# Kernel optimization log

Measured on AMD Instinct MI355X. Metric: run time of the kernel, lower is better.

## Reference

```python
import jax, jax.numpy as jnp
import numpy as np

BN_EPS = 1e-3  # keras BatchNormalization default epsilon


def setup_inputs() -> dict:
    key = jax.random.key(0)
    ks = jax.random.split(key, 7)
    B, W, D, H, C = 2, 32, 32, 32, 256
    x = jax.random.normal(ks[0], (B, W, D, H, C), dtype=jnp.float32)
    # Stacked params for the 4 branches: [query, key, judge, value]
    conv_w = jax.random.normal(ks[1], (4, C, C), dtype=jnp.float32) / np.sqrt(C).astype(np.float32)
    conv_b = jax.random.normal(ks[2], (4, C), dtype=jnp.float32) * 0.01
    bn_scale = 1.0 + 0.1 * jax.random.normal(ks[3], (4, C), dtype=jnp.float32)
    bn_offset = 0.1 * jax.random.normal(ks[4], (4, C), dtype=jnp.float32)
    bn_mean = 0.1 * jax.random.normal(ks[5], (4, C), dtype=jnp.float32)
    bn_var = jax.random.uniform(ks[6], (4, C), dtype=jnp.float32, minval=0.5, maxval=1.5)
    gamma = jnp.asarray(1e-4, dtype=jnp.float32)  # scalar residual scale (init 0.0001 in source)
    return dict(x=x, conv_w=conv_w, conv_b=conv_b, bn_scale=bn_scale,
                bn_offset=bn_offset, bn_mean=bn_mean, bn_var=bn_var, gamma=gamma)


def _branch(x, w, b, s, o, m, v):
    # Conv3D 1x1x1 == per-voxel channel mixing, then inference-mode BN, then ReLU
    y = jnp.einsum('bwdhc,cf->bwdhf', x, w) + b
    y = s * (y - m) * jax.lax.rsqrt(v + BN_EPS) + o
    return jax.nn.relu(y)


def reference(x, conv_w, conv_b, bn_scale, bn_offset, bn_mean, bn_var, gamma):
    B, W, D, H, C = x.shape
    N = W * D * H
    # Raw reshape (B,W,D,H,C) -> (B,C,N), matching keras Reshape((C,-1)) on channels-last layout
    def br(i):
        return _branch(x, conv_w[i], conv_b[i], bn_scale[i], bn_offset[i],
                       bn_mean[i], bn_var[i]).reshape(B, C, N)
    Q, K, J, V = br(0), br(1), br(2), br(3)
    m1 = jnp.matmul(K, jnp.swapaxes(Q, 1, 2))   # (B, C, C)
    m2 = jnp.matmul(K, jnp.swapaxes(J, 1, 2))   # (B, C, C)
    affinity = jax.nn.sigmoid(jnp.matmul(m1, m2))  # (B, C, C), sigmoid not softmax
    weights = jnp.matmul(affinity, V)           # (B, C, N)
    weights = weights.reshape(B, W, D, H, C)    # raw reshape back, as in source
    return gamma * weights + x
```

## Files before the change

### kernel.cpp

```cpp
#include <hip/hip_runtime.h>
#include <math.h>

typedef __attribute__((ext_vector_type(4))) float  f32x4;
typedef __attribute__((ext_vector_type(8))) short  s16x8;
typedef __attribute__((ext_vector_type(4))) short  s16x4;

#define BN_EPS 1e-3f

static constexpr int    CC    = 256;
static constexpr int    NVOX  = 32768;
static constexpr int    BATCH = 2;
static constexpr int    MTOT  = BATCH * NVOX;
static constexpr size_t ELEM_BR = (size_t)MTOT * CC;
static constexpr size_t SZ_BR   = ELEM_BR * 2;
static constexpr size_t WS_Q   = 0;
static constexpr size_t WS_K   = WS_Q  + SZ_BR;
static constexpr size_t WS_J   = WS_K  + SZ_BR;
static constexpr size_t WS_V   = WS_J  + SZ_BR;
static constexpr size_t WS_M1  = WS_V  + SZ_BR;
static constexpr size_t WS_M2  = WS_M1 + (size_t)BATCH*CC*CC*4;
static constexpr size_t WS_AFF = WS_M2 + (size_t)BATCH*CC*CC*4;
static constexpr size_t WS_WT  = WS_AFF + (size_t)BATCH*CC*CC*2;
static constexpr size_t WS_AB  = WS_WT + (size_t)4*CC*CC*2;

__device__ __forceinline__ short f2bf(float f) {
  union { float f; unsigned u; } v; v.f = f;
  unsigned u = v.u + 0x7FFFu + ((v.u >> 16) & 1u);
  return (short)(u >> 16);
}

__global__ __launch_bounds__(256) void k0_prep(
    const float* __restrict__ conv_w, const float* __restrict__ conv_b,
    const float* __restrict__ bn_s, const float* __restrict__ bn_o,
    const float* __restrict__ bn_m, const float* __restrict__ bn_v,
    char* __restrict__ ws)
{
  int t = blockIdx.x * 256 + threadIdx.x;
  ((float*)(ws + WS_M1))[t] = 0.f;
  int f = t >> 16, rem = t & 65535;
  int cin = rem >> 8, cout = rem & 255;
  ((short*)(ws + WS_WT))[f*65536 + cout*256 + cin] = f2bf(conv_w[t]);
  if (t < 1024) {
    float alpha = bn_s[t] * rsqrtf(bn_v[t] + BN_EPS);
    float beta  = alpha * (conv_b[t] - bn_m[t]) + bn_o[t];
    float* ab = (float*)(ws + WS_AB);
    ab[t] = alpha; ab[1024 + t] = beta;
  }
}

__global__ __launch_bounds__(256, 2) void k1_branches(
    const float* __restrict__ x, char* __restrict__ ws)
{
  __shared__ short As[64 * 256];
  __shared__ short Bs[64 * 256];
  __shared__ short Rs[64][72];

  const int tid = threadIdx.x;
  const int m0  = blockIdx.x * 64;
  const int lane = tid & 63, wid = tid >> 6;
  const int wm = wid >> 1, wn = wid & 1;
  const int lr = lane & 15, lg = lane >> 4;

  const short* Wt = (const short*)(ws + WS_WT);
  const float* ab = (const float*)(ws + WS_AB);

  #pragma unroll
  for (int it = 0; it < 16; ++it) {
    int idx = tid + 256 * it;
    int r = idx >> 6, c4 = (idx & 63) << 2;
    const float4 v = *(const float4*)(x + (size_t)(m0 + r) * 256 + c4);
    s16x4 s; s[0]=f2bf(v.x); s[1]=f2bf(v.y); s[2]=f2bf(v.z); s[3]=f2bf(v.w);
    int u = c4 >> 3;
    int swz = ((u ^ ((r & 7) << 2)) << 3) | (c4 & 7);
    *(s16x4*)&As[r * 256 + swz] = s;
  }

  {
    const short* Wf = Wt;
    #pragma unroll
    for (int i = 0; i < 8; ++i) {
      int slot = i * 256 + tid;
      int cout = slot >> 5, u = slot & 31;
      int usrc = u ^ ((cout & 7) << 2);
      const short* src = Wf + cout * 256 + usrc * 8;
      short* dst = Bs + (size_t)(i * 256 + wid * 64) * 8;
      __builtin_amdgcn_global_load_lds(
          (const __attribute__((address_space(1))) void*)src,
          (__attribute__((address_space(3))) void*)dst, 16, 0, 0);
    }
  }

  __syncthreads();

  for (int nt = 0; nt < 16; ++nt) {
    const int f  = nt >> 2;
    const int c0 = (nt & 3) * 64;

    f32x4 acc[2][2];
    #pragma unroll
    for (int a = 0; a < 2; ++a)
      #pragma unroll
      for (int b = 0; b < 2; ++b) { f32x4 z = {0.f,0.f,0.f,0.f}; acc[a][b] = z; }

    #pragma unroll
    for (int k0 = 0; k0 < 8; ++k0) {
      const int ua = k0 * 4 + lg;
      s16x8 af[2], bf[2];
      #pragma unroll
      for (int mi = 0; mi < 2; ++mi) {
        int r = wm*32 + mi*16 + lr;
        int uu = ua ^ ((r & 7) << 2);
        af[mi] = *(const s16x8*)&As[r * 256 + uu * 8];
      }
      #pragma unroll
      for (int nj = 0; nj < 2; ++nj) {
        int c = wn*32 + nj*16 + lr;
        int uu = ua ^ ((c & 7) << 2);
        bf[nj] = *(const s16x8*)&Bs[c * 256 + uu * 8];
      }
      #pragma unroll
      for (int mi = 0; mi < 2; ++mi)
        #pragma unroll
        for (int nj = 0; nj < 2; ++nj)
          acc[mi][nj] = __builtin_amdgcn_mfma_f32_16x16x32_bf16(
              bf[nj], af[mi], acc[mi][nj], 0, 0, 0);
    }

    __syncthreads();

    if (nt < 15) {
      const int fn  = (nt + 1) >> 2;
      const int c0n = ((nt + 1) & 3) * 64;
      const short* Wf = Wt + fn * 65536 + c0n * 256;
      #pragma unroll
      for (int i = 0; i < 8; ++i) {
        int slot = i * 256 + tid;
        int cout = slot >> 5, u = slot & 31;
        int usrc = u ^ ((cout & 7) << 2);
        const short* src = Wf + cout * 256 + usrc * 8;
        short* dst = Bs + (size_t)(i * 256 + wid * 64) * 8;
        __builtin_amdgcn_global_load_lds(
            (const __attribute__((address_space(1))) void*)src,
            (__attribute__((address_space(3))) void*)dst, 16, 0, 0);
      }
    }

    #pragma unroll
    for (int nj = 0; nj < 2; ++nj) {
      int c4b = c0 + wn*32 + nj*16 + lg*4;
      const f32x4 al = *(const f32x4*)&ab[f*256 + c4b];
      const f32x4 be = *(const f32x4*)&ab[1024 + f*256 + c4b];
      #pragma unroll
      for (int mi = 0; mi < 2; ++mi) {
        s16x4 s;
        #pragma unroll
        for (int ii = 0; ii < 4; ++ii) {
          float yv = al[ii] * acc[mi][nj][ii] + be[ii];
          yv = yv > 0.f ? yv : 0.f;
          s[ii] = f2bf(yv);
        }
        *(s16x4*)&Rs[wm*32 + mi*16 + lr][wn*32 + nj*16 + lg*4] = s;
      }
    }

    __syncthreads();

    short* Yf = (short*)(ws + (size_t)f * SZ_BR);
    #pragma unroll
    for (int it = 0; it < 2; ++it) {
      int idx = tid + 256 * it;
      int r = idx >> 3, c8 = (idx & 7) << 3;
      *(s16x8*)&Yf[(size_t)(m0 + r) * 256 + c0 + c8] = *(const s16x8*)&Rs[r][c8];
    }
  }
}

__global__ __launch_bounds__(256, 2) void k2_m1m2(char* __restrict__ ws)
{
  __shared__ short Ks[128][88], Qs[128][88], Js[128][88];

  const int tid = threadIdx.x;
  const int chunk = blockIdx.x;
  const int ti = blockIdx.y >> 1, tj = blockIdx.y & 1;
  const int b  = blockIdx.z;
  const size_t boff = (size_t)b * NVOX * CC;
  const short* Qm = (const short*)(ws + WS_Q) + boff;
  const short* Km = (const short*)(ws + WS_K) + boff;
  const short* Jm = (const short*)(ws + WS_J) + boff;

  const int lane = tid & 63, wid = tid >> 6;
  const int wm = wid >> 1, wn = wid & 1;
  const int lr = lane & 15, lg = lane >> 4;

  f32x4 accq[4][4], accj[4][4];
  #pragma unroll
  for (int a = 0; a < 4; ++a)
    #pragma unroll
    for (int c = 0; c < 4; ++c) { f32x4 z = {0.f,0.f,0.f,0.f}; accq[a][c] = z; accj[a][c] = z; }

  const int nstart = chunk * 1024;
  for (int n0 = nstart; n0 < nstart + 1024; n0 += 64) {
    __syncthreads();
    #pragma unroll
    for (int it = 0; it < 4; ++it) {
      int idx = tid + 256 * it;
      int r = idx >> 3, n8 = (idx & 7) << 3;
      *(s16x8*)&Ks[r][n8] = *(const s16x8*)&Km[(size_t)(ti*128 + r)*NVOX + n0 + n8];
      *(s16x8*)&Qs[r][n8] = *(const s16x8*)&Qm[(size_t)(tj*128 + r)*NVOX + n0 + n8];
      *(s16x8*)&Js[r][n8] = *(const s16x8*)&Jm[(size_t)(tj*128 + r)*NVOX + n0 + n8];
    }
    __syncthreads();
    #pragma unroll
    for (int ks = 0; ks < 2; ++ks) {
      s16x8 a[4], bq[4], bj[4];
      #pragma unroll
      for (int mi = 0; mi < 4; ++mi)
        a[mi] = *(const s16x8*)&Ks[wm*64 + mi*16 + lr][ks*32 + lg*8];
      #pragma unroll
      for (int nj = 0; nj < 4; ++nj) {
        bq[nj] = *(const s16x8*)&Qs[wn*64 + nj*16 + lr][ks*32 + lg*8];
        bj[nj] = *(const s16x8*)&Js[wn*64 + nj*16 + lr][ks*32 + lg*8];
      }
      #pragma unroll
      for (int mi = 0; mi < 4; ++mi)
        #pragma unroll
        for (int nj = 0; nj < 4; ++nj) {
          accq[mi][nj] = __builtin_amdgcn_mfma_f32_16x16x32_bf16(a[mi], bq[nj], accq[mi][nj], 0,0,0);
          accj[mi][nj] = __builtin_amdgcn_mfma_f32_16x16x32_bf16(a[mi], bj[nj], accj[mi][nj], 0,0,0);
        }
    }
  }
  float* m1 = (float*)(ws + WS_M1) + (size_t)b * CC * CC;
  float* m2 = (float*)(ws + WS_M2) + (size_t)b * CC * CC;
  #pragma unroll
  for (int mi = 0; mi < 4; ++mi)
    #pragma unroll
    for (int nj = 0; nj < 4; ++nj)
      #pragma unroll
      for (int ii = 0; ii < 4; ++ii) {
        int i = ti*128 + wm*64 + mi*16 + lg*4 + ii;
        int j = tj*128 + wn*64 + nj*16 + lr;
        atomicAdd(&m1[i*256 + j], accq[mi][nj][ii]);
        atomicAdd(&m2[i*256 + j], accj[mi][nj][ii]);
      }
}

__global__ __launch_bounds__(256) void k3_aff(char* __restrict__ ws)
{
  const int j = threadIdx.x;
  const int i = blockIdx.x & 255;
  const int b = blockIdx.x >> 8;
  const float* m1 = (const float*)(ws + WS_M1) + (size_t)b * CC * CC;
  const float* m2 = (const float*)(ws + WS_M2) + (size_t)b * CC * CC;
  float z = 0.f;
  #pragma unroll 8
  for (int k = 0; k < 256; ++k)
    z = fmaf(m1[i*256 + k], m2[k*256 + j], z);
  float a = 1.f / (1.f + expf(-z));
  ((short*)(ws + WS_AFF))[(size_t)b*CC*CC + i*256 + j] = f2bf(a);
}

__global__ __launch_bounds__(512, 4) void k4_out(
    const float* __restrict__ x, const float* __restrict__ gamma_p,
    char* __restrict__ ws, float* __restrict__ out)
{
  __shared__ short affS[256][72];
  __shared__ short Vs[128][72];

  const int tid = threadIdx.x;
  const int n0 = blockIdx.x * 128;
  const int b  = blockIdx.y;
  const float gamma = gamma_p[0];
  const short* aff = (const short*)(ws + WS_AFF) + (size_t)b * CC * CC;
  const short* Vm  = (const short*)(ws + WS_V) + (size_t)b * NVOX * CC;

  const int lane = tid & 63, wid = tid >> 6;
  const int wi = wid >> 1, wn = wid & 1;
  const int lr = lane & 15, lg = lane >> 4;

  f32x4 acc[4][4];
  #pragma unroll
  for (int a = 0; a < 4; ++a)
    #pragma unroll
    for (int c = 0; c < 4; ++c) { f32x4 z = {0.f,0.f,0.f,0.f}; acc[a][c] = z; }

  for (int c0 = 0; c0 < 256; c0 += 64) {
    __syncthreads();
    #pragma unroll
    for (int it = 0; it < 4; ++it) {
      int idx = tid + 512 * it;
      int r = idx >> 3, c8 = (idx & 7) << 3;
      *(s16x8*)&affS[r][c8] = *(const s16x8*)&aff[(size_t)r * 256 + c0 + c8];
    }
    #pragma unroll
    for (int it = 0; it < 2; ++it) {
      int idx = tid + 512 * it;
      int t15 = idx & 15;
      int cc = idx >> 4, n8 = t15 << 3;
      s16x8 v = *(const s16x8*)&Vm[(size_t)(c0 + cc) * NVOX + n0 + n8];
      #pragma unroll
      for (int uu = 0; uu < 8; ++uu) {
        int u = (uu + t15) & 7;
        Vs[n8 + u][cc] = v[u];
      }
    }
    __syncthreads();
    #pragma unroll
    for (int ks = 0; ks < 2; ++ks) {
      s16x8 af[4], bv[4];
      #pragma unroll
      for (int mi = 0; mi < 4; ++mi)
        af[mi] = *(const s16x8*)&affS[wi*64 + mi*16 + lr][ks*32 + lg*8];
      #pragma unroll
      for (int nj = 0; nj < 4; ++nj)
        bv[nj] = *(const s16x8*)&Vs[wn*64 + nj*16 + lr][ks*32 + lg*8];
      #pragma unroll
      for (int mi = 0; mi < 4; ++mi)
        #pragma unroll
        for (int nj = 0; nj < 4; ++nj)
          acc[mi][nj] = __builtin_amdgcn_mfma_f32_16x16x32_bf16(
              bv[nj], af[mi], acc[mi][nj], 0, 0, 0);
    }
  }
  #pragma unroll
  for (int mi = 0; mi < 4; ++mi)
    #pragma unroll
    for (int nj = 0; nj < 4; ++nj) {
      int i = wi*64 + mi*16 + lr;
      int n = n0 + wn*64 + nj*16 + lg*4;
      size_t flat = (size_t)b * NVOX * CC + (size_t)i * NVOX + n;
      const float4 xv = *(const float4*)(x + flat);
      float4 o;
      o.x = gamma * acc[mi][nj][0] + xv.x;
      o.y = gamma * acc[mi][nj][1] + xv.y;
      o.z = gamma * acc[mi][nj][2] + xv.z;
      o.w = gamma * acc[mi][nj][3] + xv.w;
      *(float4*)(out + flat) = o;
    }
}

extern "C" void kernel_launch(void* const* d_in, const int* in_sizes, int n_in,
                              void* d_out, int out_size, void* d_ws, size_t ws_size,
                              hipStream_t stream)
{
  const float* x      = (const float*)d_in[0];
  const float* conv_w = (const float*)d_in[1];
  const float* conv_b = (const float*)d_in[2];
  const float* bn_s   = (const float*)d_in[3];
  const float* bn_o   = (const float*)d_in[4];
  const float* bn_m   = (const float*)d_in[5];
  const float* bn_v   = (const float*)d_in[6];
  const float* gamma  = (const float*)d_in[7];
  char*  ws  = (char*)d_ws;
  float* out = (float*)d_out;

  k0_prep    <<<1024, 256, 0, stream>>>(conv_w, conv_b, bn_s, bn_o, bn_m, bn_v, ws);
  k1_branches<<<1024, 256, 0, stream>>>(x, ws);
  k2_m1m2    <<<dim3(32, 4, 2), 256, 0, stream>>>(ws);
  k3_aff     <<<512, 256, 0, stream>>>(ws);
  k4_out     <<<dim3(256, 2), 512, 0, stream>>>(x, gamma, ws, out);
}
```

Before: 182.7 us.

## Keep x fragments in registers and double-buffer weight tiles in k1

The branch GEMM kernel now loads each wave's x rows straight from global memory into registers as bf16 MFMA fragments, so the As staging buffer is gone. Weight tiles shrink to 32 output channels and are double-buffered in LDS, which leaves one barrier per tile instead of two. Outputs go directly to global memory as 8-byte stores rather than through an Rs staging tile. The smaller LDS footprint lets the launch bound ask for 3 blocks per CU, at the cost of more registers held for fragments and narrower, less coalesced output stores.

```diff
diff --git a/kernel.cpp b/kernel.cpp
--- a/kernel.cpp
+++ b/kernel.cpp
@@ -48,12 +48,10 @@
   }
 }
 
-__global__ __launch_bounds__(256, 2) void k1_branches(
+__global__ __launch_bounds__(256, 3) void k1_branches(
     const float* __restrict__ x, char* __restrict__ ws)
 {
-  __shared__ short As[64 * 256];
-  __shared__ short Bs[64 * 256];
-  __shared__ short Rs[64][72];
+  __shared__ short Bs[2][32 * 256];
 
   const int tid = threadIdx.x;
   const int m0  = blockIdx.x * 64;
@@ -65,113 +63,84 @@
   const float* ab = (const float*)(ws + WS_AB);
 
   #pragma unroll
-  for (int it = 0; it < 16; ++it) {
-    int idx = tid + 256 * it;
-    int r = idx >> 6, c4 = (idx & 63) << 2;
-    const float4 v = *(const float4*)(x + (size_t)(m0 + r) * 256 + c4);
-    s16x4 s; s[0]=f2bf(v.x); s[1]=f2bf(v.y); s[2]=f2bf(v.z); s[3]=f2bf(v.w);
-    int u = c4 >> 3;
-    int swz = ((u ^ ((r & 7) << 2)) << 3) | (c4 & 7);
-    *(s16x4*)&As[r * 256 + swz] = s;
-  }
-
-  {
-    const short* Wf = Wt;
-    #pragma unroll
-    for (int i = 0; i < 8; ++i) {
-      int slot = i * 256 + tid;
-      int cout = slot >> 5, u = slot & 31;
-      int usrc = u ^ ((cout & 7) << 2);
-      const short* src = Wf + cout * 256 + usrc * 8;
-      short* dst = Bs + (size_t)(i * 256 + wid * 64) * 8;
-      __builtin_amdgcn_global_load_lds(
-          (const __attribute__((address_space(1))) void*)src,
-          (__attribute__((address_space(3))) void*)dst, 16, 0, 0);
+  for (int i = 0; i < 4; ++i) {
+    int slot = i * 256 + tid;
+    int cout = slot >> 5, u = slot & 31;
+    int usrc = u ^ ((cout & 7) << 2);
+    __builtin_amdgcn_global_load_lds(
+        (const __attribute__((address_space(1))) void*)(Wt + cout * 256 + usrc * 8),
+        (__attribute__((address_space(3))) void*)(Bs[0] + (i * 256 + wid * 64) * 8),
+        16, 0, 0);
+  }
+
+  s16x8 af[2][8];
+  #pragma unroll
+  for (int mi = 0; mi < 2; ++mi) {
+    const float* xr = x + (size_t)(m0 + wm*32 + mi*16 + lr) * 256 + lg * 8;
+    #pragma unroll
+    for (int k0 = 0; k0 < 8; ++k0) {
+      const float4 v0 = *(const float4*)(xr + k0*32);
+      const float4 v1 = *(const float4*)(xr + k0*32 + 4);
+      s16x8 t;
+      t[0]=f2bf(v0.x); t[1]=f2bf(v0.y); t[2]=f2bf(v0.z); t[3]=f2bf(v0.w);
+      t[4]=f2bf(v1.x); t[5]=f2bf(v1.y); t[6]=f2bf(v1.z); t[7]=f2bf(v1.w);
+      af[mi][k0] = t;
     }
   }
 
   __syncthreads();
 
-  for (int nt = 0; nt < 16; ++nt) {
-    const int f  = nt >> 2;
-    const int c0 = (nt & 3) * 64;
-
-    f32x4 acc[2][2];
-    #pragma unroll
-    for (int a = 0; a < 2; ++a)
-      #pragma unroll
-      for (int b = 0; b < 2; ++b) { f32x4 z = {0.f,0.f,0.f,0.f}; acc[a][b] = z; }
-
-    #pragma unroll
-    for (int k0 = 0; k0 < 8; ++k0) {
-      const int ua = k0 * 4 + lg;
-      s16x8 af[2], bf[2];
-      #pragma unroll
-      for (int mi = 0; mi < 2; ++mi) {
-        int r = wm*32 + mi*16 + lr;
-        int uu = ua ^ ((r & 7) << 2);
-        af[mi] = *(const s16x8*)&As[r * 256 + uu * 8];
-      }
-      #pragma unroll
-      for (int nj = 0; nj < 2; ++nj) {
-        int c = wn*32 + nj*16 + lr;
-        int uu = ua ^ ((c & 7) << 2);
-        bf[nj] = *(const s16x8*)&Bs[c * 256 + uu * 8];
-      }
-      #pragma unroll
-      for (int mi = 0; mi < 2; ++mi)
-        #pragma unroll
-        for (int nj = 0; nj < 2; ++nj)
-          acc[mi][nj] = __builtin_amdgcn_mfma_f32_16x16x32_bf16(
-              bf[nj], af[mi], acc[mi][nj], 0, 0, 0);
-    }
-
-    __syncthreads();
-
-    if (nt < 15) {
-      const int fn  = (nt + 1) >> 2;
-      const int c0n = ((nt + 1) & 3) * 64;
-      const short* Wf = Wt + fn * 65536 + c0n * 256;
-      #pragma unroll
-      for (int i = 0; i < 8; ++i) {
+  for (int nt = 0; nt < 32; ++nt) {
+    const int f  = nt >> 3;
+    const int c0 = (nt & 7) * 32;
+    const short* BsCur = Bs[nt & 1];
+
+    if (nt < 31) {
+      const int ntn = nt + 1;
+      const short* Wf = Wt + (ntn >> 3) * 65536 + ((ntn & 7) * 32) * 256;
+      short* BsNxt = Bs[ntn & 1];
+      #pragma unroll
+      for (int i = 0; i < 4; ++i) {
         int slot = i * 256 + tid;
         int cout = slot >> 5, u = slot & 31;
         int usrc = u ^ ((cout & 7) << 2);
-        const short* src = Wf + cout * 256 + usrc * 8;
-        short* dst = Bs + (size_t)(i * 256 + wid * 64) * 8;
         __builtin_amdgcn_global_load_lds(
-            (const __attribute__((address_space(1))) void*)src,
-            (__attribute__((address_space(3))) void*)dst, 16, 0, 0);
-      }
-    }
-
-    #pragma unroll
-    for (int nj = 0; nj < 2; ++nj) {
-      int c4b = c0 + wn*32 + nj*16 + lg*4;
-      const f32x4 al = *(const f32x4*)&ab[f*256 + c4b];
-      const f32x4 be = *(const f32x4*)&ab[1024 + f*256 + c4b];
-      #pragma unroll
-      for (int mi = 0; mi < 2; ++mi) {
-        s16x4 s;
-        #pragma unroll
-        for (int ii = 0; ii < 4; ++ii) {
-          float yv = al[ii] * acc[mi][nj][ii] + be[ii];
-          yv = yv > 0.f ? yv : 0.f;
-          s[ii] = f2bf(yv);
-        }
-        *(s16x4*)&Rs[wm*32 + mi*16 + lr][wn*32 + nj*16 + lg*4] = s;
-      }
-    }
-
-    __syncthreads();
-
+            (const __attribute__((address_space(1))) void*)(Wf + cout * 256 + usrc * 8),
+            (__attribute__((address_space(3))) void*)(BsNxt + (i * 256 + wid * 64) * 8),
+            16, 0, 0);
+      }
+    }
+
+    f32x4 acc[2];
+    { f32x4 z = {0.f,0.f,0.f,0.f}; acc[0] = z; acc[1] = z; }
+    #pragma unroll
+    for (int k0 = 0; k0 < 8; ++k0) {
+      const int ua = k0 * 4 + lg;
+      const int c  = wn * 16 + lr;
+      const int uu = ua ^ ((c & 7) << 2);
+      const s16x8 bf = *(const s16x8*)&BsCur[c * 256 + uu * 8];
+      acc[0] = __builtin_amdgcn_mfma_f32_16x16x32_bf16(bf, af[0][k0], acc[0], 0, 0, 0);
+      acc[1] = __builtin_amdgcn_mfma_f32_16x16x32_bf16(bf, af[1][k0], acc[1], 0, 0, 0);
+    }
+
+    const int c4b = c0 + wn*16 + lg*4;
+    const f32x4 al = *(const f32x4*)&ab[f*256 + c4b];
+    const f32x4 be = *(const f32x4*)&ab[1024 + f*256 + c4b];
     short* Yf = (short*)(ws + (size_t)f * SZ_BR);
     #pragma unroll
-    for (int it = 0; it < 2; ++it) {
-      int idx = tid + 256 * it;
-      int r = idx >> 3, c8 = (idx & 7) << 3;
-      *(s16x8*)&Yf[(size_t)(m0 + r) * 256 + c0 + c8] = *(const s16x8*)&Rs[r][c8];
-    }
+    for (int mi = 0; mi < 2; ++mi) {
+      const int m = m0 + wm*32 + mi*16 + lr;
+      s16x4 s;
+      #pragma unroll
+      for (int ii = 0; ii < 4; ++ii) {
+        float yv = al[ii] * acc[mi][ii] + be[ii];
+        yv = yv > 0.f ? yv : 0.f;
+        s[ii] = f2bf(yv);
+      }
+      *(s16x4*)&Yf[(size_t)m * 256 + c4b] = s;
+    }
+
+    __syncthreads();
   }
 }
 
```

New measurement: 199.5 us. 1.09x slower.

## Load m1/m2 tiles via direct global-to-LDS with XOR swizzle, double grid chunks

Applied to the files above, without the earlier changes.

The K/Q/J tile staging in the m1/m2 kernel now uses direct global-to-LDS DMA loads instead of going through registers. The padded LDS rows are replaced by a dense layout with an XOR swizzle to avoid bank conflicts. The N-reduction is split into 64 chunks of 512 instead of 32 chunks of 1024, so twice as many blocks run. The goal is to hide load latency and raise occupancy, at the cost of more partial results to combine and reliance on the swizzle matching the per-wave LDS write order.

```diff
diff --git a/kernel.cpp b/kernel.cpp
--- a/kernel.cpp
+++ b/kernel.cpp
@@ -177,16 +177,18 @@
 
 __global__ __launch_bounds__(256, 2) void k2_m1m2(char* __restrict__ ws)
 {
-  __shared__ short Ks[128][88], Qs[128][88], Js[128][88];
+  __shared__ short Ks[128 * 64];
+  __shared__ short Qs[128 * 64];
+  __shared__ short Js[128 * 64];
 
   const int tid = threadIdx.x;
   const int chunk = blockIdx.x;
   const int ti = blockIdx.y >> 1, tj = blockIdx.y & 1;
   const int b  = blockIdx.z;
   const size_t boff = (size_t)b * NVOX * CC;
-  const short* Qm = (const short*)(ws + WS_Q) + boff;
-  const short* Km = (const short*)(ws + WS_K) + boff;
-  const short* Jm = (const short*)(ws + WS_J) + boff;
+  const short* Km = (const short*)(ws + WS_K) + boff + (size_t)(ti*128) * NVOX;
+  const short* Qm = (const short*)(ws + WS_Q) + boff + (size_t)(tj*128) * NVOX;
+  const short* Jm = (const short*)(ws + WS_J) + boff + (size_t)(tj*128) * NVOX;
 
   const int lane = tid & 63, wid = tid >> 6;
   const int wm = wid >> 1, wn = wid & 1;
@@ -198,28 +200,43 @@
     #pragma unroll
     for (int c = 0; c < 4; ++c) { f32x4 z = {0.f,0.f,0.f,0.f}; accq[a][c] = z; accj[a][c] = z; }
 
-  const int nstart = chunk * 1024;
-  for (int n0 = nstart; n0 < nstart + 1024; n0 += 64) {
-    __syncthreads();
-    #pragma unroll
-    for (int it = 0; it < 4; ++it) {
-      int idx = tid + 256 * it;
-      int r = idx >> 3, n8 = (idx & 7) << 3;
-      *(s16x8*)&Ks[r][n8] = *(const s16x8*)&Km[(size_t)(ti*128 + r)*NVOX + n0 + n8];
-      *(s16x8*)&Qs[r][n8] = *(const s16x8*)&Qm[(size_t)(tj*128 + r)*NVOX + n0 + n8];
-      *(s16x8*)&Js[r][n8] = *(const s16x8*)&Jm[(size_t)(tj*128 + r)*NVOX + n0 + n8];
+  for (int t = 0; t < 8; ++t) {
+    const int n0 = chunk * 512 + t * 64;
+    __syncthreads();
+    #pragma unroll
+    for (int i = 0; i < 4; ++i) {
+      int slot = i * 256 + tid;
+      int r = slot >> 3, u = slot & 7;
+      int usrc = u ^ (r & 7);
+      const size_t so = (size_t)r * NVOX + n0 + usrc * 8;
+      short* dK = Ks + (size_t)(i * 256 + wid * 64) * 8;
+      short* dQ = Qs + (size_t)(i * 256 + wid * 64) * 8;
+      short* dJ = Js + (size_t)(i * 256 + wid * 64) * 8;
+      __builtin_amdgcn_global_load_lds(
+          (const __attribute__((address_space(1))) void*)(Km + so),
+          (__attribute__((address_space(3))) void*)dK, 16, 0, 0);
+      __builtin_amdgcn_global_load_lds(
+          (const __attribute__((address_space(1))) void*)(Qm + so),
+          (__attribute__((address_space(3))) void*)dQ, 16, 0, 0);
+      __builtin_amdgcn_global_load_lds(
+          (const __attribute__((address_space(1))) void*)(Jm + so),
+          (__attribute__((address_space(3))) void*)dJ, 16, 0, 0);
     }
     __syncthreads();
     #pragma unroll
     for (int ks = 0; ks < 2; ++ks) {
+      const int ua = ks * 4 + lg;
       s16x8 a[4], bq[4], bj[4];
       #pragma unroll
-      for (int mi = 0; mi < 4; ++mi)
-        a[mi] = *(const s16x8*)&Ks[wm*64 + mi*16 + lr][ks*32 + lg*8];
+      for (int mi = 0; mi < 4; ++mi) {
+        int r = wm*64 + mi*16 + lr;
+        a[mi] = *(const s16x8*)&Ks[r * 64 + (ua ^ (r & 7)) * 8];
+      }
       #pragma unroll
       for (int nj = 0; nj < 4; ++nj) {
-        bq[nj] = *(const s16x8*)&Qs[wn*64 + nj*16 + lr][ks*32 + lg*8];
-        bj[nj] = *(const s16x8*)&Js[wn*64 + nj*16 + lr][ks*32 + lg*8];
+        int r = wn*64 + nj*16 + lr;
+        bq[nj] = *(const s16x8*)&Qs[r * 64 + (ua ^ (r & 7)) * 8];
+        bj[nj] = *(const s16x8*)&Js[r * 64 + (ua ^ (r & 7)) * 8];
       }
       #pragma unroll
       for (int mi = 0; mi < 4; ++mi)
@@ -356,7 +373,7 @@
 
   k0_prep    <<<1024, 256, 0, stream>>>(conv_w, conv_b, bn_s, bn_o, bn_m, bn_v, ws);
   k1_branches<<<1024, 256, 0, stream>>>(x, ws);
-  k2_m1m2    <<<dim3(32, 4, 2), 256, 0, stream>>>(ws);
+  k2_m1m2    <<<dim3(64, 4, 2), 256, 0, stream>>>(ws);
   k3_aff     <<<512, 256, 0, stream>>>(ws);
   k4_out     <<<dim3(256, 2), 512, 0, stream>>>(x, gamma, ws, out);
 }
```

Result: slower. 198.0 us (+8.4%).
